# Performance work log

Measured on AMD Instinct MI355X. Metric: run time of the kernel, lower is better.

## Reference

```python
import jax, jax.numpy as jnp
import numpy as np

GD, D, S, L = 14, 128, 16, 2  # gaussian_dim, hidden_dim, d_state, num_layers


def _layernorm(x, g, b):
    m = x.mean(-1, keepdims=True)
    v = ((x - m) ** 2).mean(-1, keepdims=True)
    return (x - m) / jnp.sqrt(v + 1e-5) * g + b


def _scan_dir(x, dtW, dtb, BW, CW, Alog, Dskip):
    # x: [M, N, D]. Diagonal selective SSM, one direction.
    dt = jax.nn.softplus(x @ dtW + dtb)          # [M, N, D]
    Bm = x @ BW                                   # [M, N, S]
    Cm = x @ CW                                   # [M, N, S]
    A = -jnp.exp(Alog)                            # [D, S]

    def step(s, inp):
        x_t, dt_t, B_t, C_t = inp                 # [M,D],[M,D],[M,S],[M,S]
        s = jnp.exp(A * dt_t[:, :, None]) * s + (dt_t * x_t)[:, :, None] * B_t[:, None, :]
        y = jnp.einsum('mds,ms->md', s, C_t) + Dskip * x_t
        return s, y

    s0 = jnp.zeros((x.shape[0], D, S), x.dtype)
    _, ys = jax.lax.scan(step, s0, (x.transpose(1, 0, 2), dt.transpose(1, 0, 2),
                                    Bm.transpose(1, 0, 2), Cm.transpose(1, 0, 2)))
    return ys.transpose(1, 0, 2)                  # [M, N, D]


def setup_inputs() -> dict:
    key = jax.random.key(0)
    ks = jax.random.split(key, 20)
    N, B, P = 8, 1, 20000
    inp = {}
    inp['xyz'] = jax.random.normal(ks[0], (N, B, P, 3), jnp.float32)
    inp['scale'] = jax.random.normal(ks[1], (N, B, P, 3), jnp.float32)
    inp['rotation'] = jax.random.normal(ks[2], (N, B, P, 4), jnp.float32)
    inp['opacity'] = jax.random.normal(ks[3], (N, B, P, 1), jnp.float32)
    inp['color'] = jax.random.normal(ks[4], (N, B, P, 3), jnp.float32)
    inp['t'] = jnp.array([0.37], jnp.float32)
    inp['timestamps'] = jnp.linspace(0.0, 1.0, N, dtype=jnp.float32)

    def lin(k, i, o):
        return (jax.random.normal(k, (i, o), jnp.float32) / np.sqrt(i)).astype(jnp.float32)

    inp['in_W'] = lin(ks[5], GD, D); inp['in_b'] = jnp.zeros((D,), jnp.float32)
    inp['ln_g'] = jnp.ones((L, D), jnp.float32); inp['ln_b'] = jnp.zeros((L, D), jnp.float32)
    inp['dt_W'] = jax.random.normal(ks[6], (L, 2, D, D), jnp.float32) / np.sqrt(D)
    inp['dt_b'] = jnp.zeros((L, 2, D), jnp.float32)
    inp['B_W'] = jax.random.normal(ks[7], (L, 2, D, S), jnp.float32) / np.sqrt(D)
    inp['C_W'] = jax.random.normal(ks[8], (L, 2, D, S), jnp.float32) / np.sqrt(D)
    inp['A_log'] = jnp.log(jax.random.uniform(ks[9], (L, 2, D, S), jnp.float32, 0.5, 2.0))
    inp['D_skip'] = jnp.ones((L, 2, D), jnp.float32)
    inp['out_W'] = jax.random.normal(ks[10], (L, 2 * D, D), jnp.float32) / np.sqrt(2 * D)
    inp['out_b'] = jnp.zeros((L, D), jnp.float32)
    inp['te_W1'] = jax.random.normal(ks[11], (1, D), jnp.float32)
    inp['te_b1'] = jnp.zeros((D,), jnp.float32)
    inp['te_W2'] = jax.random.normal(ks[12], (D, D), jnp.float32) / np.sqrt(D)
    inp['te_b2'] = jnp.zeros((D,), jnp.float32)
    inp['op_W'] = jax.random.normal(ks[13], (D, GD), jnp.float32) / np.sqrt(D)
    inp['op_b'] = jnp.zeros((GD,), jnp.float32)
    return inp


def reference(xyz, scale, rotation, opacity, color, t, timestamps,
              in_W, in_b, ln_g, ln_b, dt_W, dt_b, B_W, C_W, A_log, D_skip,
              out_W, out_b, te_W1, te_b1, te_W2, te_b2, op_W, op_b):
    N, B, P = xyz.shape[0], xyz.shape[1], xyz.shape[2]
    M = B * P
    # stack frames: [N,B,P,14] -> [B*P, N, 14]
    params = jnp.concatenate([xyz, scale, rotation, opacity, color], -1)
    params = params.transpose(1, 2, 0, 3).reshape(M, N, GD)
    h = params @ in_W + in_b                      # [M, N, D]
    # sinusoidal temporal position encoding from continuous timestamps
    ts = jnp.broadcast_to(timestamps[None, :], (M, N))
    half = D // 2
    freqs = jnp.exp(-jnp.log(10000.0) * jnp.arange(half, dtype=h.dtype) / half)
    ang = ts[..., None] * freqs                   # [M, N, D/2]
    h = h + jnp.concatenate([jnp.sin(ang), jnp.cos(ang)], -1)
    # bidirectional SSM layers (pre-LN, residual)
    for l in range(L):
        xn = _layernorm(h, ln_g[l], ln_b[l])
        yf = _scan_dir(xn, dt_W[l, 0], dt_b[l, 0], B_W[l, 0], C_W[l, 0], A_log[l, 0], D_skip[l, 0])
        yb = jnp.flip(_scan_dir(jnp.flip(xn, 1), dt_W[l, 1], dt_b[l, 1], B_W[l, 1], C_W[l, 1],
                                A_log[l, 1], D_skip[l, 1]), 1)
        h = h + jnp.concatenate([yf, yb], -1) @ out_W[l] + out_b[l]
    # temporal query: linear interpolation between neighboring hidden states
    t_full = jnp.broadcast_to(t.reshape(B, 1), (B, P)).reshape(M)
    tn = t_full * (N - 1)
    idx_low = jnp.clip(jnp.floor(tn).astype(jnp.int32), 0, N - 2)
    idx_high = jnp.minimum(idx_low + 1, N - 1)
    alpha = (tn - idx_low.astype(h.dtype))[:, None]
    rows = jnp.arange(M)
    h_low = h[rows, idx_low]                      # [M, D]
    h_high = h[rows, idx_high]
    h_i = (1.0 - alpha) * h_low + alpha * h_high
    te = jax.nn.silu(t_full[:, None] @ te_W1 + te_b1) @ te_W2 + te_b2
    h_i = h_i + te
    out = (h_i @ op_W + op_b).reshape(B, P, GD)
    xyz_o = out[..., :3]
    scale_o = jax.nn.softplus(out[..., 3:6])
    rot = out[..., 6:10]
    rot_o = rot / jnp.clip(jnp.linalg.norm(rot, axis=-1, keepdims=True), 1e-12)
    opac_o = jax.nn.sigmoid(out[..., 10:11])
    col_o = jax.nn.sigmoid(out[..., 11:14])
    # dict fields concatenated in canonical order -> [B, P, 14]
    return jnp.concatenate([xyz_o, scale_o, rot_o, opac_o, col_o], -1)
```

## Files before the change

kernel.cpp:

```cpp
#include <hip/hip_runtime.h>
#include <math.h>

#define DD   128
#define SS   16
#define NL   2
#define GDIM 14
#define NN   8

typedef short  s16x8 __attribute__((ext_vector_type(8)));
typedef float  f32x4 __attribute__((ext_vector_type(4)));
typedef unsigned short ushort_t;

#define WS_INW   0
#define WS_DTW   4096
#define WS_BCW   69632
#define WS_OUTW  86016
#define WS_USH   151552
#define WS_AFLT  8192
#define WS_PEB   8192
#define WS_TE    9216

#if __has_builtin(__builtin_amdgcn_exp2f)
#define EXP2(x) __builtin_amdgcn_exp2f(x)
#else
#define EXP2(x) exp2f(x)
#endif

__device__ __forceinline__ unsigned short f2bf(float f) {
    unsigned u = __float_as_uint(f);
    u += 0x7fffu + ((u >> 16) & 1u);
    return (unsigned short)(u >> 16);
}

__device__ __forceinline__ float softplus_fast(float x) {
    return fmaxf(x, 0.f) + __logf(1.f + __expf(-fabsf(x)));
}
__device__ __forceinline__ float softplus_precise(float x) {
    return fmaxf(x, 0.f) + log1pf(expf(-fabsf(x)));
}

extern "C" __global__ void __launch_bounds__(256)
prep_weights(const float* __restrict__ inW, const float* __restrict__ dtW,
             const float* __restrict__ BW,  const float* __restrict__ CW,
             const float* __restrict__ outW, const float* __restrict__ Alog,
             const float* __restrict__ tstamp, const float* __restrict__ inB,
             const float* __restrict__ t_arr,
             const float* __restrict__ teW1, const float* __restrict__ teB1,
             const float* __restrict__ teW2, const float* __restrict__ teB2,
             int Bcnt, ushort_t* __restrict__ ws)
{
    float* wsf = (float*)(ws + WS_USH);
    int i = blockIdx.x * 256 + threadIdx.x;
    if (i < 4096) {
        int d = i >> 5, k = i & 31;
        ws[WS_INW + i] = (k < GDIM) ? f2bf(inW[k * DD + d]) : (ushort_t)0;
        return;
    }
    i -= 4096;
    if (i < 65536) {
        int l = i >> 15, r = i & 32767;
        int col = r >> 7, k = r & 127;
        int dir = col >> 7, d = col & 127;
        ws[WS_DTW + i] = f2bf(dtW[((size_t)(l * 2 + dir) * DD + k) * DD + d]);
        return;
    }
    i -= 65536;
    if (i < 16384) {
        int l = i >> 13, r = i & 8191;
        int col = r >> 7, k = r & 127;
        int dir = col >> 5, which = (col >> 4) & 1, s = col & 15;
        const float* Wsrc = which ? CW : BW;
        ws[WS_BCW + i] = f2bf(Wsrc[((size_t)(l * 2 + dir) * DD + k) * SS + s]);
        return;
    }
    i -= 16384;
    if (i < 65536) {
        int l = i >> 15, r = i & 32767;
        int col = r >> 8, k = r & 255;
        ws[WS_OUTW + i] = f2bf(outW[((size_t)l * 2 * DD + k) * DD + col]);
        return;
    }
    i -= 65536;
    if (i < WS_AFLT) {
        int ld = i >> 11, r = i & 2047;
        int s = r >> 7, d = r & 127;
        wsf[i] = -expf(Alog[((size_t)ld * DD + d) * SS + s]) * 1.44269504088896f;
        return;
    }
    i -= WS_AFLT;
    if (i < 1024) {
        int n = i >> 7, d = i & 127;
        int j = d & 63;
        float freq = expf(-logf(10000.f) * (float)j * (1.f / 64.f));
        float ang = tstamp[n] * freq;
        wsf[WS_PEB + i] = inB[d] + ((d < 64) ? sinf(ang) : cosf(ang));
        return;
    }
    i -= 1024;
    if (i < Bcnt * 128) {
        int b = i >> 7, d = i & 127;
        float tv = t_arr[b];
        float acc = teB2[d];
        for (int k = 0; k < DD; ++k) {
            float u = fmaf(tv, teW1[k], teB1[k]);
            float s = u / (1.f + expf(-u));
            acc = fmaf(s, teW2[k * DD + d], acc);
        }
        wsf[WS_TE + i] = acc;
    }
}

extern "C" __global__ void __launch_bounds__(256, 4)
ssm_mfma(const float* __restrict__ xyz, const float* __restrict__ scl,
         const float* __restrict__ rotp, const float* __restrict__ opa,
         const float* __restrict__ colp,
         const float* __restrict__ t_arr,
         const float* __restrict__ lnG, const float* __restrict__ lnB,
         const float* __restrict__ dtB,
         const float* __restrict__ Dskp,
         const float* __restrict__ outB,
         const float* __restrict__ opW, const float* __restrict__ opB,
         const ushort_t* __restrict__ wsu,
         float* __restrict__ out, int M, int Pb)
{
    const int t    = threadIdx.x;
    const int lane = t & 63;
    const int wv   = t >> 6;
    const int d    = t & 127;
    const int p    = t >> 7;
    const int m0   = blockIdx.x * 2;
    const int m    = m0 + p;
    const int r16  = lane & 15;
    const int kg   = lane >> 4;

    __shared__ float arenaA[16][132];
    __shared__ float arenaB[16][260];
    __shared__ float red  [4][2][NN];

    float (*pres)[132] = arenaA;
    ushort_t* XsU = (ushort_t*)&arenaA[0][0];
    float (*bcres)[68] = (float(*)[68])&arenaA[0][0];
    float (*dtres)[260] = arenaB;
    ushort_t* YsU = (ushort_t*)&arenaB[0][0];

    const ushort_t* inWt  = wsu + WS_INW;
    const ushort_t* dtWt  = wsu + WS_DTW;
    const ushort_t* bcWt  = wsu + WS_BCW;
    const ushort_t* outWt = wsu + WS_OUTW;
    const float*    wsf   = (const float*)(wsu + WS_USH);
    const float*    Apre  = wsf;
    const float*    peb   = wsf + WS_PEB;
    const float*    te    = wsf + WS_TE;

    for (int idx = t; idx < 16 * 32; idx += 256) {
        const int row = idx >> 5, k = idx & 31;
        const int pp = row >> 3, n = row & 7;
        const int mm = m0 + pp;
        float v = 0.f;
        if (k < GDIM && mm < M) {
            if (k < 3)       v = xyz [((size_t)n * M + mm) * 3 + k];
            else if (k < 6)  v = scl [((size_t)n * M + mm) * 3 + (k - 3)];
            else if (k < 10) v = rotp[((size_t)n * M + mm) * 4 + (k - 6)];
            else if (k < 11) v = opa [ (size_t)n * M + mm];
            else             v = colp[((size_t)n * M + mm) * 3 + (k - 11)];
        }
        XsU[row * 264 + k] = f2bf(v);
    }
    __syncthreads();

    {
        const s16x8 a = *(const s16x8*)&XsU[r16 * 264 + kg * 8];
        __syncthreads();
        #pragma unroll
        for (int ti = 0; ti < 2; ++ti) {
            const int col = (wv * 2 + ti) * 16 + r16;
            const s16x8 b = *(const s16x8*)&inWt[col * 32 + kg * 8];
            f32x4 acc = {0.f, 0.f, 0.f, 0.f};
            acc = __builtin_amdgcn_mfma_f32_16x16x32_bf16(a, b, acc, 0, 0, 0);
            #pragma unroll
            for (int j = 0; j < 4; ++j) pres[kg * 4 + j][col] = acc[j];
        }
    }
    __syncthreads();

    float h[NN];
    #pragma unroll
    for (int n = 0; n < NN; ++n)
        h[n] = pres[p * 8 + n][d] + peb[n * DD + d];

    for (int l = 0; l < NL; ++l) {
        float sum[NN], sq[NN];
        #pragma unroll
        for (int n = 0; n < NN; ++n) { sum[n] = h[n]; sq[n] = h[n] * h[n]; }
        #pragma unroll
        for (int off = 32; off > 0; off >>= 1) {
            #pragma unroll
            for (int n = 0; n < NN; ++n) {
                sum[n] += __shfl_xor(sum[n], off);
                sq[n]  += __shfl_xor(sq[n],  off);
            }
        }
        if (lane == 0) {
            #pragma unroll
            for (int n = 0; n < NN; ++n) { red[wv][0][n] = sum[n]; red[wv][1][n] = sq[n]; }
        }
        __syncthreads();

        float xn[NN];
        {
            const float gg = lnG[l * DD + d], bb = lnB[l * DD + d];
            #pragma unroll
            for (int n = 0; n < NN; ++n) {
                const float s0 = red[2 * p][0][n] + red[2 * p + 1][0][n];
                const float s1 = red[2 * p][1][n] + red[2 * p + 1][1][n];
                const float mean = s0 * (1.f / 128.f);
                float var = s1 * (1.f / 128.f) - mean * mean;
                const float inv = rsqrtf(fmaxf(var, 0.f) + 1e-5f);
                xn[n] = fmaf((h[n] - mean) * inv, gg, bb);
                XsU[(p * 8 + n) * 264 + d] = f2bf(xn[n]);
            }
        }
        __syncthreads();

        {
            s16x8 a[4];
            #pragma unroll
            for (int kc = 0; kc < 4; ++kc)
                a[kc] = *(const s16x8*)&XsU[r16 * 264 + kc * 32 + kg * 8];
            __syncthreads();

            const ushort_t* dtl = dtWt + l * 32768;
            #pragma unroll
            for (int ti = 0; ti < 4; ++ti) {
                const int col = (wv * 4 + ti) * 16 + r16;
                f32x4 acc = {0.f, 0.f, 0.f, 0.f};
                #pragma unroll
                for (int kc = 0; kc < 4; ++kc) {
                    const s16x8 b = *(const s16x8*)&dtl[col * 128 + kc * 32 + kg * 8];
                    acc = __builtin_amdgcn_mfma_f32_16x16x32_bf16(a[kc], b, acc, 0, 0, 0);
                }
                #pragma unroll
                for (int j = 0; j < 4; ++j) dtres[kg * 4 + j][col] = acc[j];
            }
            const ushort_t* bcl = bcWt + l * 8192;
            {
                const int col = wv * 16 + r16;
                f32x4 acc = {0.f, 0.f, 0.f, 0.f};
                #pragma unroll
                for (int kc = 0; kc < 4; ++kc) {
                    const s16x8 b = *(const s16x8*)&bcl[col * 128 + kc * 32 + kg * 8];
                    acc = __builtin_amdgcn_mfma_f32_16x16x32_bf16(a[kc], b, acc, 0, 0, 0);
                }
                #pragma unroll
                for (int j = 0; j < 4; ++j) bcres[kg * 4 + j][col] = acc[j];
            }
        }
        __syncthreads();

        float dtv[2][NN];
        #pragma unroll
        for (int dir = 0; dir < 2; ++dir) {
            const float db = dtB[(l * 2 + dir) * DD + d];
            #pragma unroll
            for (int n = 0; n < NN; ++n)
                dtv[dir][n] = softplus_fast(dtres[p * 8 + n][dir * 128 + d] + db);
        }
        __syncthreads();

        #pragma unroll
        for (int dir = 0; dir < 2; ++dir) {
            const float* Ap = Apre + (size_t)(l * 2 + dir) * SS * DD + d;
            float Ar[SS];
            #pragma unroll
            for (int s = 0; s < SS; ++s) Ar[s] = Ap[s * DD];
            const float dsk = Dskp[(l * 2 + dir) * DD + d];
            float st[SS];
            #pragma unroll
            for (int s = 0; s < SS; ++s) st[s] = 0.f;
            #pragma unroll
            for (int t8 = 0; t8 < NN; ++t8) {
                const int n = dir ? (NN - 1 - t8) : t8;
                const float dtc = dtv[dir][n];
                const float xv  = xn[n];
                const float dx  = dtc * xv;
                float y = dsk * xv;
                const float* base = &bcres[p * 8 + n][dir * 32];
                #pragma unroll
                for (int s4 = 0; s4 < SS; s4 += 4) {
                    const float4 Bv = *(const float4*)&base[s4];
                    const float4 Cv = *(const float4*)&base[16 + s4];
                    st[s4+0] = fmaf(EXP2(Ar[s4+0] * dtc), st[s4+0], dx * Bv.x);
                    y = fmaf(st[s4+0], Cv.x, y);
                    st[s4+1] = fmaf(EXP2(Ar[s4+1] * dtc), st[s4+1], dx * Bv.y);
                    y = fmaf(st[s4+1], Cv.y, y);
                    st[s4+2] = fmaf(EXP2(Ar[s4+2] * dtc), st[s4+2], dx * Bv.z);
                    y = fmaf(st[s4+2], Cv.z, y);
                    st[s4+3] = fmaf(EXP2(Ar[s4+3] * dtc), st[s4+3], dx * Bv.w);
                    y = fmaf(st[s4+3], Cv.w, y);
                }
                YsU[(p * 8 + n) * 520 + dir * 128 + d] = f2bf(y);
            }
        }
        __syncthreads();

        {
            s16x8 a[8];
            #pragma unroll
            for (int kc = 0; kc < 8; ++kc)
                a[kc] = *(const s16x8*)&YsU[r16 * 520 + kc * 32 + kg * 8];
            const ushort_t* ol = outWt + l * 32768;
            #pragma unroll
            for (int ti = 0; ti < 2; ++ti) {
                const int col = (wv * 2 + ti) * 16 + r16;
                f32x4 acc = {0.f, 0.f, 0.f, 0.f};
                #pragma unroll
                for (int kc = 0; kc < 8; ++kc) {
                    const s16x8 b = *(const s16x8*)&ol[col * 256 + kc * 32 + kg * 8];
                    acc = __builtin_amdgcn_mfma_f32_16x16x32_bf16(a[kc], b, acc, 0, 0, 0);
                }
                #pragma unroll
                for (int j = 0; j < 4; ++j) pres[kg * 4 + j][col] = acc[j];
            }
        }
        __syncthreads();

        {
            const float ob = outB[l * DD + d];
            #pragma unroll
            for (int n = 0; n < NN; ++n) h[n] += pres[p * 8 + n][d] + ob;
        }
    }

    const int mc = (m < M) ? m : (M - 1);
    const int bidx = mc / Pb;
    const float tv = t_arr[bidx];
    const float tn = tv * (float)(NN - 1);
    int il = (int)floorf(tn);
    il = il < 0 ? 0 : (il > NN - 2 ? NN - 2 : il);
    const float alpha = tn - (float)il;
    float hlow = 0.f, hhigh = 0.f;
    #pragma unroll
    for (int n = 0; n < NN; ++n) {
        if (n == il)     hlow  = h[n];
        if (n == il + 1) hhigh = h[n];
    }
    float hi = (1.f - alpha) * hlow + alpha * hhigh + te[bidx * DD + d];

    float* epi = &arenaB[0][0];
    epi[p * 132 + d] = hi;
    __syncthreads();

    if (d < GDIM * 8) {
        const int g = d >> 3, j = d & 7;
        float part = 0.f;
        #pragma unroll
        for (int q = 0; q < 16; ++q)
            part = fmaf(epi[p * 132 + j + 8 * q], opW[(j + 8 * q) * GDIM + g], part);
        part += __shfl_xor(part, 4);
        part += __shfl_xor(part, 2);
        part += __shfl_xor(part, 1);
        if (j == 0) epi[264 + p * 16 + g] = part + opB[g];
    }
    __syncthreads();

    if (d < GDIM && m < M) {
        const int g = d;
        const float v = epi[264 + p * 16 + g];
        float r;
        if (g < 3)        r = v;
        else if (g < 6)   r = softplus_precise(v);
        else if (g < 10) {
            const float q0 = epi[264 + p * 16 + 6], q1 = epi[264 + p * 16 + 7];
            const float q2 = epi[264 + p * 16 + 8], q3 = epi[264 + p * 16 + 9];
            const float nrm = sqrtf(fmaf(q0,q0, fmaf(q1,q1, fmaf(q2,q2, q3*q3))));
            r = v / fmaxf(nrm, 1e-12f);
        } else {
            r = 1.f / (1.f + expf(-v));
        }
        out[(size_t)m * GDIM + g] = r;
    }
}

extern "C" void kernel_launch(void* const* d_in, const int* in_sizes, int n_in,
                              void* d_out, int out_size, void* d_ws, size_t ws_size,
                              hipStream_t stream) {
    const float* xyz   = (const float*)d_in[0];
    const float* scl   = (const float*)d_in[1];
    const float* rotp  = (const float*)d_in[2];
    const float* opa   = (const float*)d_in[3];
    const float* colp  = (const float*)d_in[4];
    const float* t_arr = (const float*)d_in[5];
    const float* tstmp = (const float*)d_in[6];
    const float* inW   = (const float*)d_in[7];
    const float* inB   = (const float*)d_in[8];
    const float* lnG   = (const float*)d_in[9];
    const float* lnB   = (const float*)d_in[10];
    const float* dtW   = (const float*)d_in[11];
    const float* dtB   = (const float*)d_in[12];
    const float* BW    = (const float*)d_in[13];
    const float* CW    = (const float*)d_in[14];
    const float* Alog  = (const float*)d_in[15];
    const float* Dskp  = (const float*)d_in[16];
    const float* outW  = (const float*)d_in[17];
    const float* outB  = (const float*)d_in[18];
    const float* teW1  = (const float*)d_in[19];
    const float* teB1  = (const float*)d_in[20];
    const float* teW2  = (const float*)d_in[21];
    const float* teB2  = (const float*)d_in[22];
    const float* opW   = (const float*)d_in[23];
    const float* opB   = (const float*)d_in[24];

    const int N  = in_sizes[6];
    const int M  = in_sizes[3] / N;
    const int B  = in_sizes[5];
    const int Pb = M / B;
    (void)out_size; (void)n_in;

    ushort_t* wsu = (ushort_t*)d_ws;
    const int prep_elems = WS_USH + WS_AFLT + 1024 + B * 128;
    hipLaunchKernelGGL(prep_weights, dim3((prep_elems + 255) / 256), dim3(256), 0, stream,
                       inW, dtW, BW, CW, outW, Alog, tstmp, inB, t_arr,
                       teW1, teB1, teW2, teB2, B, wsu);
    hipLaunchKernelGGL(ssm_mfma, dim3((M + 1) / 2), dim3(256), 0, stream,
                       xyz, scl, rotp, opa, colp, t_arr,
                       lnG, lnB, dtB, Dskp, outB, opW, opB,
                       wsu, (float*)d_out, M, Pb);
}
```

Baseline: 491.0 us.

## Split SSM scan into two state halves to cut registers and double occupancy

Raises the launch-bounds occupancy hint from 4 to 8 waves per SIMD. To fit that register budget, the selective scan now runs each direction as two passes over 8 state channels each instead of holding all 16, carrying the partial y per timestep between passes. Softplus dt values are computed per direction rather than for both at once. The trade is more redundant LDS reads and loop overhead, and the tighter register cap could force spills.

```diff
diff --git a/kernel.cpp b/kernel.cpp
--- a/kernel.cpp
+++ b/kernel.cpp
@@ -110,7 +110,7 @@
     }
 }
 
-extern "C" __global__ void __launch_bounds__(256, 4)
+extern "C" __global__ void __launch_bounds__(256, 8)
 ssm_mfma(const float* __restrict__ xyz, const float* __restrict__ scl,
          const float* __restrict__ rotp, const float* __restrict__ opa,
          const float* __restrict__ colp,
@@ -257,49 +257,51 @@
         }
         __syncthreads();
 
-        float dtv[2][NN];
         #pragma unroll
         for (int dir = 0; dir < 2; ++dir) {
-            const float db = dtB[(l * 2 + dir) * DD + d];
+            float dtv8[NN];
+            {
+                const float db = dtB[(l * 2 + dir) * DD + d];
+                #pragma unroll
+                for (int n = 0; n < NN; ++n)
+                    dtv8[n] = softplus_fast(dtres[p * 8 + n][dir * 128 + d] + db);
+            }
+            if (dir == 0) __syncthreads();
+            const float dsk = Dskp[(l * 2 + dir) * DD + d];
+            const float* Ap = Apre + (size_t)(l * 2 + dir) * SS * DD + d;
+            float y[NN];
+            #pragma unroll
+            for (int half = 0; half < 2; ++half) {
+                float Ar[8], st[8];
+                #pragma unroll
+                for (int j = 0; j < 8; ++j) { Ar[j] = Ap[(half * 8 + j) * DD]; st[j] = 0.f; }
+                #pragma unroll
+                for (int t8 = 0; t8 < NN; ++t8) {
+                    const int n = dir ? (NN - 1 - t8) : t8;
+                    const float dtc = dtv8[n];
+                    const float xv  = xn[n];
+                    const float dx  = dtc * xv;
+                    float yy = half ? y[n] : dsk * xv;
+                    const float* base = &bcres[p * 8 + n][dir * 32 + half * 8];
+                    #pragma unroll
+                    for (int s4 = 0; s4 < 8; s4 += 4) {
+                        const float4 Bv = *(const float4*)&base[s4];
+                        const float4 Cv = *(const float4*)&base[16 + s4];
+                        st[s4+0] = fmaf(EXP2(Ar[s4+0] * dtc), st[s4+0], dx * Bv.x);
+                        yy = fmaf(st[s4+0], Cv.x, yy);
+                        st[s4+1] = fmaf(EXP2(Ar[s4+1] * dtc), st[s4+1], dx * Bv.y);
+                        yy = fmaf(st[s4+1], Cv.y, yy);
+                        st[s4+2] = fmaf(EXP2(Ar[s4+2] * dtc), st[s4+2], dx * Bv.z);
+                        yy = fmaf(st[s4+2], Cv.z, yy);
+                        st[s4+3] = fmaf(EXP2(Ar[s4+3] * dtc), st[s4+3], dx * Bv.w);
+                        yy = fmaf(st[s4+3], Cv.w, yy);
+                    }
+                    y[n] = yy;
+                }
+            }
             #pragma unroll
             for (int n = 0; n < NN; ++n)
-                dtv[dir][n] = softplus_fast(dtres[p * 8 + n][dir * 128 + d] + db);
-        }
-        __syncthreads();
-
-        #pragma unroll
-        for (int dir = 0; dir < 2; ++dir) {
-            const float* Ap = Apre + (size_t)(l * 2 + dir) * SS * DD + d;
-            float Ar[SS];
-            #pragma unroll
-            for (int s = 0; s < SS; ++s) Ar[s] = Ap[s * DD];
-            const float dsk = Dskp[(l * 2 + dir) * DD + d];
-            float st[SS];
-            #pragma unroll
-            for (int s = 0; s < SS; ++s) st[s] = 0.f;
-            #pragma unroll
-            for (int t8 = 0; t8 < NN; ++t8) {
-                const int n = dir ? (NN - 1 - t8) : t8;
-                const float dtc = dtv[dir][n];
-                const float xv  = xn[n];
-                const float dx  = dtc * xv;
-                float y = dsk * xv;
-                const float* base = &bcres[p * 8 + n][dir * 32];
-                #pragma unroll
-                for (int s4 = 0; s4 < SS; s4 += 4) {
-                    const float4 Bv = *(const float4*)&base[s4];
-                    const float4 Cv = *(const float4*)&base[16 + s4];
-                    st[s4+0] = fmaf(EXP2(Ar[s4+0] * dtc), st[s4+0], dx * Bv.x);
-                    y = fmaf(st[s4+0], Cv.x, y);
-                    st[s4+1] = fmaf(EXP2(Ar[s4+1] * dtc), st[s4+1], dx * Bv.y);
-                    y = fmaf(st[s4+1], Cv.y, y);
-                    st[s4+2] = fmaf(EXP2(Ar[s4+2] * dtc), st[s4+2], dx * Bv.z);
-                    y = fmaf(st[s4+2], Cv.z, y);
-                    st[s4+3] = fmaf(EXP2(Ar[s4+3] * dtc), st[s4+3], dx * Bv.w);
-                    y = fmaf(st[s4+3], Cv.w, y);
-                }
-                YsU[(p * 8 + n) * 520 + dir * 128 + d] = f2bf(y);
-            }
+                YsU[(p * 8 + n) * 520 + dir * 128 + d] = f2bf(y[n]);
         }
         __syncthreads();
 
```

After: 550.9 us. +12.2%, slower.
